# Optimization experiments

Hardware: AMD Instinct MI355X
Metric: run time of the kernel (lower is better)

## Reference

```python
import jax, jax.numpy as jnp
import numpy as np

CHW = (1, 256, 256)
NPH, NPW = 16, 16
NB = 8          # n_blocks
D = 384         # hidden_d
H = 6           # n_heads
DH = D // H     # d_head = 64
OUT = 4
PH, PW = CHW[1] // NPH, CHW[2] // NPW
IN_D = CHW[0] * PH * PW        # 256
S = NPH * NPW + 1              # 257 tokens (CLS + patches)
EPS = 1e-5                     # torch LayerNorm default


def positional_embeddings(seq_len, d):
    # matches get_positional_embeddings: sin(i/10000^(j/d)) even j, cos(i/10000^((j-1)/d)) odd j
    i = jnp.arange(seq_len, dtype=jnp.float32)[:, None]
    j = jnp.arange(d, dtype=jnp.float32)[None, :]
    j_eff = jnp.where(j % 2 == 0, j, j - 1)
    ang = i / jnp.power(jnp.float32(10000.0), j_eff / d)
    return jnp.where(j % 2 == 0, jnp.sin(ang), jnp.cos(ang))


def patchify(images):
    # (n,c,h,w) -> (n, NPH*NPW, c*PH*PW), patch flattened channel-first like patch.flatten()
    n, c, h, w = images.shape
    x = images.reshape(n, c, NPH, PH, NPW, PW)
    x = x.transpose(0, 2, 4, 1, 3, 5)  # n, nph, npw, c, ph, pw
    return x.reshape(n, NPH * NPW, c * PH * PW)


def layernorm(x, g, b):
    mu = jnp.mean(x, axis=-1, keepdims=True)
    var = jnp.mean(jnp.square(x - mu), axis=-1, keepdims=True)
    return (x - mu) * jax.lax.rsqrt(var + EPS) * g + b


def mhsa(x, Wq, bq, Wk, bk, Wv, bv):
    # x: [B,S,D]; W*: [H,DH,DH] (torch Linear convention out=x@W.T+b), b*: [H,DH]
    B = x.shape[0]
    xh = x.reshape(B, S, H, DH)
    q = jnp.einsum('bshd,hed->bshe', xh, Wq) + bq
    k = jnp.einsum('bshd,hed->bshe', xh, Wk) + bk
    v = jnp.einsum('bshd,hed->bshe', xh, Wv) + bv
    scores = jnp.einsum('bqhe,bkhe->bhqk', q, k) / jnp.float32(DH) ** 0.5
    attn = jax.nn.softmax(scores, axis=-1)
    o = jnp.einsum('bhqk,bkhe->bqhe', attn, v)
    return o.reshape(B, S, D)


def setup_inputs() -> dict:
    key = jax.random.key(0)
    ks = jax.random.split(key, 24)
    s = 0.02
    B = 64
    inp = {
        'images': jax.random.normal(ks[0], (B, *CHW), jnp.float32),
        'Wmap': jax.random.normal(ks[1], (D, IN_D), jnp.float32) * s,
        'bmap': jax.random.normal(ks[2], (D,), jnp.float32) * s,
        'cls': jax.random.uniform(ks[3], (1, D), jnp.float32),
        'ln1_g': jnp.ones((NB, D), jnp.float32),
        'ln1_b': jnp.zeros((NB, D), jnp.float32),
        'Wq': jax.random.normal(ks[4], (NB, H, DH, DH), jnp.float32) * s,
        'bq': jax.random.normal(ks[5], (NB, H, DH), jnp.float32) * s,
        'Wk': jax.random.normal(ks[6], (NB, H, DH, DH), jnp.float32) * s,
        'bk': jax.random.normal(ks[7], (NB, H, DH), jnp.float32) * s,
        'Wv': jax.random.normal(ks[8], (NB, H, DH, DH), jnp.float32) * s,
        'bv': jax.random.normal(ks[9], (NB, H, DH), jnp.float32) * s,
        'ln2_g': jnp.ones((NB, D), jnp.float32),
        'ln2_b': jnp.zeros((NB, D), jnp.float32),
        'W1': jax.random.normal(ks[10], (NB, 4 * D, D), jnp.float32) * s,
        'b1': jax.random.normal(ks[11], (NB, 4 * D), jnp.float32) * s,
        'W2': jax.random.normal(ks[12], (NB, D, 4 * D), jnp.float32) * s,
        'b2': jax.random.normal(ks[13], (NB, D), jnp.float32) * s,
        'Wout': jax.random.normal(ks[14], (OUT, D), jnp.float32) * s,
        'bout': jax.random.normal(ks[15], (OUT,), jnp.float32) * s,
    }
    return inp


def reference(images, Wmap, bmap, cls, ln1_g, ln1_b, Wq, bq, Wk, bk, Wv, bv,
              ln2_g, ln2_b, W1, b1, W2, b2, Wout, bout):
    B = images.shape[0]
    patches = patchify(images)                        # [B, S-1, IN_D]
    tokens = patches @ Wmap.T + bmap                  # [B, S-1, D]
    tokens = jnp.concatenate([jnp.broadcast_to(cls[None], (B, 1, D)), tokens], axis=1)
    out = tokens + positional_embeddings(S, D)[None]  # [B, S, D]
    for blk in range(NB):
        out = out + mhsa(layernorm(out, ln1_g[blk], ln1_b[blk]),
                         Wq[blk], bq[blk], Wk[blk], bk[blk], Wv[blk], bv[blk])
        h = layernorm(out, ln2_g[blk], ln2_b[blk])
        h = jax.nn.gelu(h @ W1[blk].T + b1[blk], approximate=False)
        out = out + (h @ W2[blk].T + b2[blk])
    cls_out = out[:, 0]                               # [B, D]
    return jax.nn.softmax(cls_out @ Wout.T + bout, axis=-1)
```

## Files before the change

kernel.cpp:

```cpp
#include <hip/hip_runtime.h>

typedef __bf16 bf16x8 __attribute__((ext_vector_type(8)));
typedef float f32x4 __attribute__((ext_vector_type(4)));
typedef unsigned short u16;
typedef unsigned short u16x4 __attribute__((ext_vector_type(4)));

typedef __attribute__((address_space(3))) unsigned int as3_u32;
typedef __attribute__((address_space(1))) unsigned int as1_u32;

static __device__ __forceinline__ float b2f(u16 u) {
    union { unsigned int ui; float f; } v; v.ui = ((unsigned int)u) << 16; return v.f;
}
static __device__ __forceinline__ u16 f2b(float f) {
    union { float f; unsigned int u; } v; v.f = f;
    unsigned int r = v.u + 0x7FFFu + ((v.u >> 16) & 1u);
    return (u16)(r >> 16);
}
static __device__ __forceinline__ float pos_emb(int s, int d) {
    int je = d & ~1;
    float ang = (float)s * powf(10000.0f, -(float)je / 384.0f);
    return (d & 1) ? cosf(ang) : sinf(ang);
}
static __device__ __forceinline__ float gelu_f(float x) {
    float xs = x * 0.70710678118654752f;
    float ax = fabsf(xs);
    float t = __builtin_amdgcn_rcpf(1.0f + 0.3275911f * ax);
    float poly = ((((1.061405429f * t - 1.453152027f) * t + 1.421413741f) * t
                   - 0.284496736f) * t + 0.254829592f) * t;
    float e = __expf(-ax * ax);
    float erfv = 1.0f - poly * e;
    erfv = (xs < 0.f) ? -erfv : erfv;
    return 0.5f * x * (1.0f + erfv);
}
static __device__ __forceinline__ void async16(const void* g, void* l) {
    __builtin_amdgcn_global_load_lds((const as1_u32*)g, (as3_u32*)l, 16, 0, 0);
}

#define MFMA16 __builtin_amdgcn_mfma_f32_16x16x32_bf16

template<int K>
static __device__ __forceinline__ void stage_tile(const u16* __restrict__ gbase,
                                                  u16* lds, int kt, int t) {
#pragma unroll
    for (int j = 0; j < 4; j++) {
        int o = j * 4096 + t * 16;
        int row = o >> 7;
        int c = (o >> 4) & 7;
        int gc = c ^ (row & 7);
        const u16* src = gbase + (size_t)row * K + kt * 64 + gc * 8;
        async16(src, (char*)lds + o);
    }
}

template<int K, int EPI>
__global__ __launch_bounds__(256) void k_gemm128(const u16* __restrict__ A,
                                                 const u16* __restrict__ Bw,
                                                 const float* __restrict__ bias,
                                                 u16* __restrict__ out16,
                                                 float* __restrict__ xres,
                                                 int m0g) {
    __shared__ u16 lds[2][128 * 64];
    const int t = threadIdx.x;
    const int NY = gridDim.y;
    int nwg = gridDim.x * NY;
    int flat = blockIdx.x + gridDim.x * blockIdx.y;
    int q8 = nwg >> 3, r8 = nwg & 7, xcd = flat & 7, idx = flat >> 3;
    int wg = (xcd < r8 ? xcd * (q8 + 1) : r8 * (q8 + 1) + (xcd - r8) * q8) + idx;
    const int mt = wg / NY, nt = wg - mt * NY;

    const u16* Ab = A + (size_t)mt * 128 * K;
    const u16* Bb = Bw + (size_t)nt * 128 * K;
    constexpr int NKT = K / 64;
    const int lane = t & 63, w = t >> 6;
    const int wm = (w >> 1) * 64, wn = (w & 1) * 64;
    const int r = lane & 15, g = lane >> 4;

    f32x4 acc[4][4] = {};
    for (int kt = 0; kt < NKT; kt++) {
        stage_tile<K>(Ab, lds[0], kt, t);
        stage_tile<K>(Bb, lds[1], kt, t);
        asm volatile("s_waitcnt vmcnt(0)" ::: "memory");
        __builtin_amdgcn_sched_barrier(0);
        __builtin_amdgcn_s_barrier();
        __builtin_amdgcn_sched_barrier(0);
#pragma unroll
        for (int ks = 0; ks < 2; ks++) {
            bf16x8 a[4], b[4];
#pragma unroll
            for (int i = 0; i < 4; i++) {
                int ra = wm + i * 16 + r;
                int ca = (ks * 4 + g) ^ (ra & 7);
                a[i] = *(const bf16x8*)((const char*)lds[0] + ra * 128 + ca * 16);
                int rb = wn + i * 16 + r;
                int cb = (ks * 4 + g) ^ (rb & 7);
                b[i] = *(const bf16x8*)((const char*)lds[1] + rb * 128 + cb * 16);
            }
            __builtin_amdgcn_s_setprio(1);
#pragma unroll
            for (int i = 0; i < 4; i++)
#pragma unroll
                for (int jj = 0; jj < 4; jj++)
                    acc[i][jj] = MFMA16(a[i], b[jj], acc[i][jj], 0, 0, 0);
            __builtin_amdgcn_s_setprio(0);
        }
        __builtin_amdgcn_s_barrier();
    }
#pragma unroll
    for (int i = 0; i < 4; i++) {
#pragma unroll
        for (int q = 0; q < 4; q++) {
            int ml = mt * 128 + wm + i * 16 + g * 4 + q;
#pragma unroll
            for (int jj = 0; jj < 4; jj++) {
                int n = nt * 128 + wn + jj * 16 + r;
                float v = acc[i][jj][q] + bias[n];
                if (EPI == 0) {
                    out16[(size_t)ml * 1536 + n] = f2b(gelu_f(v));
                } else {
                    int m = m0g + ml;
                    if (m < 16448) xres[(size_t)m * 384 + n] += v;
                }
            }
        }
    }
}

__global__ __launch_bounds__(64) void k_fattn(const u16* __restrict__ qb,
                                              const u16* __restrict__ kb,
                                              const u16* __restrict__ vT,
                                              float* __restrict__ x) {
    __shared__ u16 pl[32][40];
    const int lane = threadIdx.x;
    int flat = blockIdx.x;
    int xcd = flat & 7, idx = flat >> 3;
    int lbh = idx / 9;
    const int bh = xcd * 48 + lbh;
    const int q0 = (idx - lbh * 9) * 32;
    const int b = bh / 6, h = bh - b * 6;
    const int r = lane & 15, g = lane >> 4;

    const u16* qbase = qb + ((size_t)b * 257) * 384 + h * 64;
    const u16* kbase = kb + ((size_t)b * 257) * 384 + h * 64;
    const u16* vbase = vT + ((size_t)bh * 64) * 288;

    bf16x8 qf[2][2];
#pragma unroll
    for (int ti = 0; ti < 2; ti++)
#pragma unroll
        for (int kh = 0; kh < 2; kh++)
            qf[ti][kh] = *(const bf16x8*)(qbase + (size_t)(q0 + ti * 16 + r) * 384 + kh * 32 + g * 8);

    f32x4 accO[2][2][2] = {};
    f32x4 sum_[2] = {};

    for (int kv0 = 0; kv0 < 288; kv0 += 32) {
        bf16x8 kf[2][2];
#pragma unroll
        for (int tj = 0; tj < 2; tj++)
#pragma unroll
            for (int kh = 0; kh < 2; kh++)
                kf[tj][kh] = *(const bf16x8*)(kbase + (size_t)(kv0 + tj * 16 + r) * 384 + kh * 32 + g * 8);
        bf16x8 vf[2][2];
#pragma unroll
        for (int eT = 0; eT < 2; eT++)
#pragma unroll
            for (int tjE = 0; tjE < 2; tjE++)
                vf[eT][tjE] = *(const bf16x8*)(vbase + (size_t)(eT * 32 + tjE * 16 + r) * 288 + kv0 + g * 8);

        f32x4 s_[2][2] = {};
#pragma unroll
        for (int ti = 0; ti < 2; ti++)
#pragma unroll
            for (int tj = 0; tj < 2; tj++) {
                s_[ti][tj] = MFMA16(qf[ti][0], kf[tj][0], s_[ti][tj], 0, 0, 0);
                s_[ti][tj] = MFMA16(qf[ti][1], kf[tj][1], s_[ti][tj], 0, 0, 0);
            }
#pragma unroll
        for (int ti = 0; ti < 2; ti++) {
#pragma unroll
            for (int tj = 0; tj < 2; tj++) {
                bool bad = (kv0 + tj * 16 + r) >= 257;
#pragma unroll
                for (int q = 0; q < 4; q++) {
                    float p = bad ? 0.f : __expf(s_[ti][tj][q] * 0.125f);
                    s_[ti][tj][q] = p;
                }
                sum_[ti] += s_[ti][tj];
#pragma unroll
                for (int q = 0; q < 4; q++)
                    pl[ti * 16 + g * 4 + q][tj * 16 + r] = f2b(s_[ti][tj][q]);
            }
        }
        bf16x8 pa[2];
#pragma unroll
        for (int ti2 = 0; ti2 < 2; ti2++)
            pa[ti2] = *(const bf16x8*)&pl[ti2 * 16 + r][g * 8];
#pragma unroll
        for (int eT = 0; eT < 2; eT++)
#pragma unroll
            for (int ti2 = 0; ti2 < 2; ti2++)
#pragma unroll
                for (int tjE = 0; tjE < 2; tjE++)
                    accO[eT][ti2][tjE] = MFMA16(pa[ti2], vf[eT][tjE], accO[eT][ti2][tjE], 0, 0, 0);
    }
#pragma unroll
    for (int o = 1; o < 16; o <<= 1)
#pragma unroll
        for (int ti = 0; ti < 2; ti++)
#pragma unroll
            for (int q = 0; q < 4; q++)
                sum_[ti][q] += __shfl_xor(sum_[ti][q], o, 64);
#pragma unroll
    for (int ti = 0; ti < 2; ti++)
#pragma unroll
        for (int q = 0; q < 4; q++) {
            int qi = q0 + ti * 16 + g * 4 + q;
            if (qi < 257) {
                float inv = 1.0f / sum_[ti][q];
                float* px = x + ((size_t)b * 257 + qi) * 384 + h * 64;
#pragma unroll
                for (int eT = 0; eT < 2; eT++)
#pragma unroll
                    for (int tjE = 0; tjE < 2; tjE++)
                        px[eT * 32 + tjE * 16 + r] += accO[eT][ti][tjE][q] * inv;
            }
        }
}

__global__ __launch_bounds__(256) void k_cvt16(const void* __restrict__ src, u16* __restrict__ dst,
                                               int n, const unsigned* __restrict__ probe) {
    const bool isf32 = (*probe == 0x3F800000u);
    int i0 = (blockIdx.x * 256 + threadIdx.x) * 4;
    if (isf32) {
        const float* s = (const float*)src;
#pragma unroll
        for (int j = 0; j < 4; j++) { int i = i0 + j; if (i < n) dst[i] = f2b(s[i]); }
    } else {
        const u16* s = (const u16*)src;
#pragma unroll
        for (int j = 0; j < 4; j++) { int i = i0 + j; if (i < n) dst[i] = s[i]; }
    }
}
__global__ __launch_bounds__(256) void k_cvt32(const void* __restrict__ src, float* __restrict__ dst,
                                               int n, const unsigned* __restrict__ probe) {
    const bool isf32 = (*probe == 0x3F800000u);
    int i0 = (blockIdx.x * 256 + threadIdx.x) * 4;
    if (isf32) {
        const float* s = (const float*)src;
#pragma unroll
        for (int j = 0; j < 4; j++) { int i = i0 + j; if (i < n) dst[i] = s[i]; }
    } else {
        const u16* s = (const u16*)src;
#pragma unroll
        for (int j = 0; j < 4; j++) { int i = i0 + j; if (i < n) dst[i] = b2f(s[i]); }
    }
}

__global__ __launch_bounds__(256) void k_vtpad(u16* __restrict__ vT) {
    int idx = blockIdx.x * 256 + threadIdx.x;
    const int total = 384 * 64 * 31;
    if (idx < total) {
        int be = idx / 31; int s = 257 + (idx - be * 31);
        vT[(size_t)be * 288 + s] = 0;
    }
}

__global__ __launch_bounds__(256) void k_patch(const u16* __restrict__ img,
                                               const u16* __restrict__ Wmap,
                                               const float* __restrict__ bmap,
                                               float* __restrict__ x) {
    const int lane = threadIdx.x & 63;
    const int wv = threadIdx.x >> 6;
    const int mt = blockIdx.x * 4 + wv;
    const int nt = blockIdx.y;
    const int m0 = mt * 32, n0 = nt * 32;
    const int r = lane & 15, kr = (lane >> 4) << 3;
    f32x4 acc[2][2] = {};
    int ma = m0 + r;
    size_t base0 = (size_t)(ma >> 8) * 65536 + (size_t)((ma >> 4) & 15) * 4096 + (size_t)(ma & 15) * 16;
    ma += 16;
    size_t base1 = (size_t)(ma >> 8) * 65536 + (size_t)((ma >> 4) & 15) * 4096 + (size_t)(ma & 15) * 16;
    const u16* pb0 = Wmap + (size_t)(n0 + r) * 256 + kr;
    const u16* pb1 = pb0 + 16 * 256;
    for (int k0 = 0; k0 < 256; k0 += 32) {
        int k = k0 + kr;
        size_t off = (size_t)(k >> 4) * 256 + (k & 15);
        bf16x8 a0 = *(const bf16x8*)(img + base0 + off);
        bf16x8 a1 = *(const bf16x8*)(img + base1 + off);
        bf16x8 b0 = *(const bf16x8*)(pb0 + k0);
        bf16x8 b1 = *(const bf16x8*)(pb1 + k0);
        acc[0][0] = MFMA16(a0, b0, acc[0][0], 0, 0, 0);
        acc[0][1] = MFMA16(a0, b1, acc[0][1], 0, 0, 0);
        acc[1][0] = MFMA16(a1, b0, acc[1][0], 0, 0, 0);
        acc[1][1] = MFMA16(a1, b1, acc[1][1], 0, 0, 0);
    }
#pragma unroll
    for (int ti = 0; ti < 2; ti++)
#pragma unroll
        for (int i = 0; i < 4; i++) {
            int m = m0 + ti * 16 + ((lane >> 4) << 2) + i;
            int b = m >> 8, p = m & 255, s = p + 1;
            float* px = x + ((size_t)b * 257 + s) * 384;
#pragma unroll
            for (int tj = 0; tj < 2; tj++) {
                int n = n0 + tj * 16 + (lane & 15);
                px[n] = acc[ti][tj][i] + bmap[n] + pos_emb(s, n);
            }
        }
}

__global__ __launch_bounds__(384) void k_cls(const float* __restrict__ cls, float* __restrict__ x) {
    int b = blockIdx.x, d = threadIdx.x;
    x[(size_t)b * 257 * 384 + d] = cls[d] + pos_emb(0, d);
}

__global__ __launch_bounds__(256) void k_ln(const float* __restrict__ x,
                                            const float* __restrict__ g,
                                            const float* __restrict__ bb,
                                            u16* __restrict__ xn) {
    const int lane = threadIdx.x & 63, wv = threadIdx.x >> 6;
    const int row = blockIdx.x * 16 + wv * 4 + (lane >> 4);
    const int r = lane & 15;
    const float* px = x + (size_t)row * 384;
    f32x4 v[6]; float s = 0.f;
#pragma unroll
    for (int i = 0; i < 6; i++) {
        v[i] = *(const f32x4*)(px + i * 64 + r * 4);
        s += v[i][0] + v[i][1] + v[i][2] + v[i][3];
    }
#pragma unroll
    for (int o = 1; o < 16; o <<= 1) s += __shfl_xor(s, o, 64);
    float mu = s * (1.0f / 384.0f);
    float q = 0.f;
#pragma unroll
    for (int i = 0; i < 6; i++)
#pragma unroll
        for (int j = 0; j < 4; j++) { float d = v[i][j] - mu; q += d * d; }
#pragma unroll
    for (int o = 1; o < 16; o <<= 1) q += __shfl_xor(q, o, 64);
    float rstd = rsqrtf(q * (1.0f / 384.0f) + 1e-5f);
    u16* po = xn + (size_t)row * 384;
#pragma unroll
    for (int i = 0; i < 6; i++) {
        int d0 = i * 64 + r * 4;
        f32x4 gg = *(const f32x4*)(g + d0);
        f32x4 bv = *(const f32x4*)(bb + d0);
        u16x4 o4;
#pragma unroll
        for (int j = 0; j < 4; j++) o4[j] = f2b((v[i][j] - mu) * rstd * gg[j] + bv[j]);
        *(u16x4*)(po + d0) = o4;
    }
}

__global__ __launch_bounds__(256) void k_qkv3(const u16* __restrict__ xn,
                                              const u16* __restrict__ Wq,
                                              const u16* __restrict__ Wk,
                                              const u16* __restrict__ Wv,
                                              const float* __restrict__ bq,
                                              const float* __restrict__ bk,
                                              const float* __restrict__ bv,
                                              u16* __restrict__ qo,
                                              u16* __restrict__ ko,
                                              u16* __restrict__ vT) {
    const int lane = threadIdx.x & 63, wv = threadIdx.x >> 6;
    int nwg = 129 * 12;
    int flat = blockIdx.x + 129 * blockIdx.y;
    int q8 = nwg >> 3, r8 = nwg & 7, xcd = flat & 7, idx = flat >> 3;
    int wg = (xcd < r8 ? xcd * (q8 + 1) : r8 * (q8 + 1) + (xcd - r8) * q8) + idx;
    int bxx = wg / 12, rest = wg - bxx * 12;

    const int mt = bxx * 4 + wv; if (mt >= 514) return;
    const int nt = rest & 1, h = rest >> 1;
    const int r = lane & 15, kr = (lane >> 4) << 3;

    const u16* Abase = xn + (size_t)(mt * 32) * 384 + h * 64;
    bf16x8 a00 = *(const bf16x8*)(Abase + (size_t)r * 384 + kr);
    bf16x8 a10 = *(const bf16x8*)(Abase + (size_t)(16 + r) * 384 + kr);
    bf16x8 a01 = *(const bf16x8*)(Abase + (size_t)r * 384 + 32 + kr);
    bf16x8 a11 = *(const bf16x8*)(Abase + (size_t)(16 + r) * 384 + 32 + kr);

    const u16* Ws[3] = { Wq, Wk, Wv };
    const float* bs[3] = { bq, bk, bv };
#pragma unroll
    for (int ty = 0; ty < 3; ty++) {
        const u16* Bb = Ws[ty] + ((size_t)h * 64 + nt * 32) * 64;
        bf16x8 b00 = *(const bf16x8*)(Bb + (size_t)r * 64 + kr);
        bf16x8 b10 = *(const bf16x8*)(Bb + (size_t)(16 + r) * 64 + kr);
        bf16x8 b01 = *(const bf16x8*)(Bb + (size_t)r * 64 + 32 + kr);
        bf16x8 b11 = *(const bf16x8*)(Bb + (size_t)(16 + r) * 64 + 32 + kr);
        f32x4 acc[2][2] = {};
        acc[0][0] = MFMA16(a00, b00, acc[0][0], 0, 0, 0);
        acc[0][1] = MFMA16(a00, b10, acc[0][1], 0, 0, 0);
        acc[1][0] = MFMA16(a10, b00, acc[1][0], 0, 0, 0);
        acc[1][1] = MFMA16(a10, b10, acc[1][1], 0, 0, 0);
        acc[0][0] = MFMA16(a01, b01, acc[0][0], 0, 0, 0);
        acc[0][1] = MFMA16(a01, b11, acc[0][1], 0, 0, 0);
        acc[1][0] = MFMA16(a11, b01, acc[1][0], 0, 0, 0);
        acc[1][1] = MFMA16(a11, b11, acc[1][1], 0, 0, 0);
        const float* bias = bs[ty];
#pragma unroll
        for (int ti = 0; ti < 2; ti++)
#pragma unroll
            for (int i = 0; i < 4; i++) {
                int m = mt * 32 + ti * 16 + ((lane >> 4) << 2) + i;
#pragma unroll
                for (int tj = 0; tj < 2; tj++) {
                    int nl = nt * 32 + tj * 16 + (lane & 15);
                    float v = acc[ti][tj][i] + bias[h * 64 + nl];
                    if (ty == 0) {
                        qo[(size_t)m * 384 + h * 64 + nl] = f2b(v);
                    } else if (ty == 1) {
                        ko[(size_t)m * 384 + h * 64 + nl] = f2b(v);
                    } else {
                        int b = m / 257, s = m - b * 257;
                        vT[(((size_t)b * 6 + h) * 64 + nl) * 288 + s] = f2b(v);
                    }
                }
            }
    }
}

__global__ __launch_bounds__(256) void k_head(const float* __restrict__ x,
                                              const float* __restrict__ Wout,
                                              const float* __restrict__ bout,
                                              float* __restrict__ out) {
    int t = threadIdx.x; int b = t >> 2, o = t & 3;
    const float* px = x + (size_t)b * 257 * 384;
    const float* pw = Wout + o * 384;
    float s = 0.f;
    for (int d = 0; d < 384; d++) s += px[d] * pw[d];
    s += bout[o];
    float mx = fmaxf(s, __shfl_xor(s, 1, 4));
    mx = fmaxf(mx, __shfl_xor(mx, 2, 4));
    float e = expf(s - mx);
    float sm = e + __shfl_xor(e, 1, 4);
    sm += __shfl_xor(sm, 2, 4);
    out[t] = e / sm;
}

extern "C" void kernel_launch(void* const* d_in, const int* in_sizes, int n_in,
                              void* d_out, int out_size, void* d_ws, size_t ws_size,
                              hipStream_t stream) {
    const unsigned* probe = (const unsigned*)d_in[4];

    char* w = (char*)d_ws;
    size_t used = 0;
    auto alloc = [&](size_t bytes) -> char* {
        char* p = w + used; used += (bytes + 255) & ~(size_t)255; return p;
    };
    float* x   = (float*)alloc(16448ull * 384 * 4);
    u16*   xn  = (u16*)  alloc(16512ull * 384 * 2);
    u16*   qb  = (u16*)  alloc((16448ull + 32) * 384 * 2);
    u16*   kb  = (u16*)  alloc((16448ull + 32) * 384 * 2);
    u16*   vT  = (u16*)  alloc(384ull * 64 * 288 * 2);
    u16*   imB = (u16*)  alloc(4194304ull * 2);
    u16*   WmB = (u16*)  alloc(98304ull * 2);
    u16*   WqB = (u16*)  alloc(196608ull * 2);
    u16*   WkB = (u16*)  alloc(196608ull * 2);
    u16*   WvB = (u16*)  alloc(196608ull * 2);
    u16*   W1B = (u16*)  alloc(4718592ull * 2);
    u16*   W2B = (u16*)  alloc(4718592ull * 2);
    float* prm = (float*)alloc(39172ull * 4);
    char*  flexp = w + used;
    size_t flex = (ws_size > used) ? (ws_size - used) : 0;

    long long ft = (long long)(flex / (128ull * 1536 * 2));
    int FT128 = (ft > 129) ? 129 : (int)ft;
    if (FT128 < 1) FT128 = 1;
    u16* hb = (u16*)flexp;

    float* bmapF = prm + 0;
    float* clsF  = prm + 384;
    float* ln1gF = prm + 768;
    float* ln1bF = prm + 3840;
    float* bqF   = prm + 6912;
    float* bkF   = prm + 9984;
    float* bvF   = prm + 13056;
    float* ln2gF = prm + 16128;
    float* ln2bF = prm + 19200;
    float* b1F   = prm + 22272;
    float* b2F   = prm + 34560;
    float* WoutF = prm + 37632;
    float* boutF = prm + 39168;

    dim3 B256(256);
    auto cvt16 = [&](const void* src, u16* dst, int n) {
        hipLaunchKernelGGL(k_cvt16, dim3((n + 1023) / 1024), B256, 0, stream, src, dst, n, probe);
    };
    auto cvt32 = [&](const void* src, float* dst, int n) {
        hipLaunchKernelGGL(k_cvt32, dim3((n + 1023) / 1024), B256, 0, stream, src, dst, n, probe);
    };
    cvt16(d_in[0],  imB, 4194304);
    cvt16(d_in[1],  WmB, 98304);
    cvt16(d_in[6],  WqB, 196608);
    cvt16(d_in[8],  WkB, 196608);
    cvt16(d_in[10], WvB, 196608);
    cvt16(d_in[14], W1B, 4718592);
    cvt16(d_in[16], W2B, 4718592);
    cvt32(d_in[2],  bmapF, 384);
    cvt32(d_in[3],  clsF,  384);
    cvt32(d_in[4],  ln1gF, 3072);
    cvt32(d_in[5],  ln1bF, 3072);
    cvt32(d_in[7],  bqF,   3072);
    cvt32(d_in[9],  bkF,   3072);
    cvt32(d_in[11], bvF,   3072);
    cvt32(d_in[12], ln2gF, 3072);
    cvt32(d_in[13], ln2bF, 3072);
    cvt32(d_in[15], b1F,   12288);
    cvt32(d_in[17], b2F,   3072);
    cvt32(d_in[18], WoutF, 1536);
    cvt32(d_in[19], boutF, 4);
    (void)in_sizes; (void)n_in; (void)out_size;

    hipMemsetAsync(xn + 16448ull * 384, 0, 64ull * 384 * 2, stream);

    hipLaunchKernelGGL(k_vtpad, dim3((384 * 64 * 31 + 255) / 256), B256, 0, stream, vT);
    hipLaunchKernelGGL(k_patch, dim3(128, 12), B256, 0, stream, imB, WmB, bmapF, x);
    hipLaunchKernelGGL(k_cls, dim3(64), dim3(384), 0, stream, clsF, x);
    for (int blk = 0; blk < 8; blk++) {
        hipLaunchKernelGGL(k_ln, dim3(1028), B256, 0, stream, x, ln1gF + blk * 384, ln1bF + blk * 384, xn);
        hipLaunchKernelGGL(k_qkv3, dim3(129, 12), B256, 0, stream, xn,
                           WqB + (size_t)blk * 24576, WkB + (size_t)blk * 24576, WvB + (size_t)blk * 24576,
                           bqF + blk * 384, bkF + blk * 384, bvF + blk * 384,
                           qb, kb, vT);
        hipLaunchKernelGGL(k_fattn, dim3(3456), dim3(64), 0, stream, qb, kb, vT, x);
        hipLaunchKernelGGL(k_ln, dim3(1028), B256, 0, stream, x, ln2gF + blk * 384, ln2bF + blk * 384, xn);
        for (int T0 = 0; T0 < 129; T0 += FT128) {
            int nt = (129 - T0 < FT128) ? (129 - T0) : FT128;
            k_gemm128<384, 0><<<dim3(nt, 12), B256, 0, stream>>>(
                xn + (size_t)T0 * 128 * 384, W1B + (size_t)blk * 1536 * 384,
                b1F + blk * 1536, hb, nullptr, 0);
            k_gemm128<1536, 1><<<dim3(nt, 3), B256, 0, stream>>>(
                hb, W2B + (size_t)blk * 384 * 1536,
                b2F + blk * 384, nullptr, x, T0 * 128);
        }
    }
    hipLaunchKernelGGL(k_head, dim3(1), B256, 0, stream, x, WoutF, boutF, (float*)d_out);
}
```

Baseline: 1.401 ms.

## Enlarge MLP GEMM tiles to 256x128 with 512 threads and LDS-staged GELU stores

```diff
diff --git a/kernel.cpp b/kernel.cpp
--- a/kernel.cpp
+++ b/kernel.cpp
@@ -4,6 +4,7 @@
 typedef float f32x4 __attribute__((ext_vector_type(4)));
 typedef unsigned short u16;
 typedef unsigned short u16x4 __attribute__((ext_vector_type(4)));
+typedef unsigned short u16x8 __attribute__((ext_vector_type(8)));
 
 typedef __attribute__((address_space(3))) unsigned int as3_u32;
 typedef __attribute__((address_space(1))) unsigned int as1_u32;
@@ -38,28 +39,16 @@
 
 #define MFMA16 __builtin_amdgcn_mfma_f32_16x16x32_bf16
 
-template<int K>
-static __device__ __forceinline__ void stage_tile(const u16* __restrict__ gbase,
-                                                  u16* lds, int kt, int t) {
-#pragma unroll
-    for (int j = 0; j < 4; j++) {
-        int o = j * 4096 + t * 16;
-        int row = o >> 7;
-        int c = (o >> 4) & 7;
-        int gc = c ^ (row & 7);
-        const u16* src = gbase + (size_t)row * K + kt * 64 + gc * 8;
-        async16(src, (char*)lds + o);
-    }
-}
-
 template<int K, int EPI>
-__global__ __launch_bounds__(256) void k_gemm128(const u16* __restrict__ A,
+__global__ __launch_bounds__(512) void k_gemm256(const u16* __restrict__ A,
                                                  const u16* __restrict__ Bw,
                                                  const float* __restrict__ bias,
                                                  u16* __restrict__ out16,
                                                  float* __restrict__ xres,
                                                  int m0g) {
-    __shared__ u16 lds[2][128 * 64];
+    __shared__ u16 lds[24576];
+    u16* ldsA = lds;
+    u16* ldsB = lds + 16384;
     const int t = threadIdx.x;
     const int NY = gridDim.y;
     int nwg = gridDim.x * NY;
@@ -68,7 +57,7 @@
     int wg = (xcd < r8 ? xcd * (q8 + 1) : r8 * (q8 + 1) + (xcd - r8) * q8) + idx;
     const int mt = wg / NY, nt = wg - mt * NY;
 
-    const u16* Ab = A + (size_t)mt * 128 * K;
+    const u16* Ab = A + (size_t)mt * 256 * K;
     const u16* Bb = Bw + (size_t)nt * 128 * K;
     constexpr int NKT = K / 64;
     const int lane = t & 63, w = t >> 6;
@@ -77,8 +66,18 @@
 
     f32x4 acc[4][4] = {};
     for (int kt = 0; kt < NKT; kt++) {
-        stage_tile<K>(Ab, lds[0], kt, t);
-        stage_tile<K>(Bb, lds[1], kt, t);
+#pragma unroll
+        for (int j = 0; j < 4; j++) {
+            int o = j * 8192 + t * 16;
+            int row = o >> 7, c = (o >> 4) & 7, gc = c ^ (row & 7);
+            async16(Ab + (size_t)row * K + kt * 64 + gc * 8, (char*)ldsA + o);
+        }
+#pragma unroll
+        for (int j = 0; j < 2; j++) {
+            int o = j * 8192 + t * 16;
+            int row = o >> 7, c = (o >> 4) & 7, gc = c ^ (row & 7);
+            async16(Bb + (size_t)row * K + kt * 64 + gc * 8, (char*)ldsB + o);
+        }
         asm volatile("s_waitcnt vmcnt(0)" ::: "memory");
         __builtin_amdgcn_sched_barrier(0);
         __builtin_amdgcn_s_barrier();
@@ -90,10 +89,10 @@
             for (int i = 0; i < 4; i++) {
                 int ra = wm + i * 16 + r;
                 int ca = (ks * 4 + g) ^ (ra & 7);
-                a[i] = *(const bf16x8*)((const char*)lds[0] + ra * 128 + ca * 16);
+                a[i] = *(const bf16x8*)((const char*)ldsA + ra * 128 + ca * 16);
                 int rb = wn + i * 16 + r;
                 int cb = (ks * 4 + g) ^ (rb & 7);
-                b[i] = *(const bf16x8*)((const char*)lds[1] + rb * 128 + cb * 16);
+                b[i] = *(const bf16x8*)((const char*)ldsB + rb * 128 + cb * 16);
             }
             __builtin_amdgcn_s_setprio(1);
 #pragma unroll
@@ -105,21 +104,52 @@
         }
         __builtin_amdgcn_s_barrier();
     }
-#pragma unroll
-    for (int i = 0; i < 4; i++) {
-#pragma unroll
-        for (int q = 0; q < 4; q++) {
-            int ml = mt * 128 + wm + i * 16 + g * 4 + q;
-#pragma unroll
-            for (int jj = 0; jj < 4; jj++) {
-                int n = nt * 128 + wn + jj * 16 + r;
-                float v = acc[i][jj][q] + bias[n];
-                if (EPI == 0) {
-                    out16[(size_t)ml * 1536 + n] = f2b(gelu_f(v));
-                } else {
-                    int m = m0g + ml;
-                    if (m < 16448) xres[(size_t)m * 384 + n] += v;
+
+    if (EPI == 1) {
+#pragma unroll
+        for (int i = 0; i < 4; i++)
+#pragma unroll
+            for (int q = 0; q < 4; q++) {
+                int ml = mt * 256 + wm + i * 16 + g * 4 + q;
+                int m = m0g + ml;
+                if (m < 16448) {
+#pragma unroll
+                    for (int jj = 0; jj < 4; jj++) {
+                        int n = nt * 128 + wn + jj * 16 + r;
+                        xres[(size_t)m * 384 + n] += acc[i][jj][q] + bias[n];
+                    }
                 }
+            }
+    } else {
+#pragma unroll
+        for (int hi = 0; hi < 2; hi++) {
+            __syncthreads();
+            if ((w >> 2) == hi) {
+                int lwm = wm - hi * 128;
+#pragma unroll
+                for (int i = 0; i < 4; i++)
+#pragma unroll
+                    for (int q = 0; q < 4; q++) {
+                        int lr = lwm + i * 16 + g * 4 + q;
+                        int xorv = (lr & 12) << 3;
+#pragma unroll
+                        for (int jj = 0; jj < 4; jj++) {
+                            int col = wn + jj * 16 + r;
+                            float v = acc[i][jj][q] + bias[nt * 128 + col];
+                            *(u16*)((char*)lds + lr * 256 + ((col * 2) ^ xorv)) =
+                                f2b(gelu_f(v));
+                        }
+                    }
+            }
+            __syncthreads();
+            int prow = t >> 2;
+            int off = (t & 3) * 64;
+            int xorv = (prow & 12) << 3;
+            size_t gbase = (size_t)(mt * 256 + hi * 128 + prow) * 1536 + nt * 128 + off / 2;
+#pragma unroll
+            for (int k2 = 0; k2 < 4; k2++) {
+                u16x8 val = *(const u16x8*)((const char*)lds + prow * 256 + ((off + 16 * k2) ^ xorv));
+                *(u16x8*)(out16 + gbase + 8 * k2) = val;
             }
         }
     }
@@ -449,7 +479,7 @@
         char* p = w + used; used += (bytes + 255) & ~(size_t)255; return p;
     };
     float* x   = (float*)alloc(16448ull * 384 * 4);
-    u16*   xn  = (u16*)  alloc(16512ull * 384 * 2);
+    u16*   xn  = (u16*)  alloc(16640ull * 384 * 2);
     u16*   qb  = (u16*)  alloc((16448ull + 32) * 384 * 2);
     u16*   kb  = (u16*)  alloc((16448ull + 32) * 384 * 2);
     u16*   vT  = (u16*)  alloc(384ull * 64 * 288 * 2);
@@ -464,9 +494,9 @@
     char*  flexp = w + used;
     size_t flex = (ws_size > used) ? (ws_size - used) : 0;
 
-    long long ft = (long long)(flex / (128ull * 1536 * 2));
-    int FT128 = (ft > 129) ? 129 : (int)ft;
-    if (FT128 < 1) FT128 = 1;
+    long long ft = (long long)(flex / (256ull * 1536 * 2));
+    int FT256 = (ft > 65) ? 65 : (int)ft;
+    if (FT256 < 1) FT256 = 1;
     u16* hb = (u16*)flexp;
 
     float* bmapF = prm + 0;
@@ -512,7 +542,7 @@
     cvt32(d_in[19], boutF, 4);
     (void)in_sizes; (void)n_in; (void)out_size;
 
-    hipMemsetAsync(xn + 16448ull * 384, 0, 64ull * 384 * 2, stream);
+    hipMemsetAsync(xn + 16448ull * 384, 0, 192ull * 384 * 2, stream);
 
     hipLaunchKernelGGL(k_vtpad, dim3((384 * 64 * 31 + 255) / 256), B256, 0, stream, vT);
     hipLaunchKernelGGL(k_patch, dim3(128, 12), B256, 0, stream, imB, WmB, bmapF, x);
@@ -525,14 +555,14 @@
                            qb, kb, vT);
         hipLaunchKernelGGL(k_fattn, dim3(3456), dim3(64), 0, stream, qb, kb, vT, x);
         hipLaunchKernelGGL(k_ln, dim3(1028), B256, 0, stream, x, ln2gF + blk * 384, ln2bF + blk * 384, xn);
-        for (int T0 = 0; T0 < 129; T0 += FT128) {
-            int nt = (129 - T0 < FT128) ? (129 - T0) : FT128;
-            k_gemm128<384, 0><<<dim3(nt, 12), B256, 0, stream>>>(
-                xn + (size_t)T0 * 128 * 384, W1B + (size_t)blk * 1536 * 384,
+        for (int T0 = 0; T0 < 65; T0 += FT256) {
+            int nt = (65 - T0 < FT256) ? (65 - T0) : FT256;
+            k_gemm256<384, 0><<<dim3(nt, 12), dim3(512), 0, stream>>>(
+                xn + (size_t)T0 * 256 * 384, W1B + (size_t)blk * 1536 * 384,
                 b1F + blk * 1536, hb, nullptr, 0);
-            k_gemm128<1536, 1><<<dim3(nt, 3), B256, 0, stream>>>(
+            k_gemm256<1536, 1><<<dim3(nt, 3), dim3(512), 0, stream>>>(
                 hb, W2B + (size_t)blk * 384 * 1536,
-                b2F + blk * 384, nullptr, x, T0 * 128);
+                b2F + blk * 384, nullptr, x, T0 * 256);
         }
     }
     hipLaunchKernelGGL(k_head, dim3(1), B256, 0, stream, x, WoutF, boutF, (float*)d_out);
```

Result: slower. 1.532 ms (+9.3%).

## Fuse FFN up-projection, GELU and down-projection into one kernel

Applied to the files above, without the earlier changes.

```diff
diff --git a/kernel.cpp b/kernel.cpp
--- a/kernel.cpp
+++ b/kernel.cpp
@@ -38,91 +38,104 @@
 
 #define MFMA16 __builtin_amdgcn_mfma_f32_16x16x32_bf16
 
-template<int K>
-static __device__ __forceinline__ void stage_tile(const u16* __restrict__ gbase,
-                                                  u16* lds, int kt, int t) {
-#pragma unroll
-    for (int j = 0; j < 4; j++) {
-        int o = j * 4096 + t * 16;
-        int row = o >> 7;
-        int c = (o >> 4) & 7;
+__global__ __launch_bounds__(512) void k_ffn(const u16* __restrict__ xn,
+                                             const u16* __restrict__ W1,
+                                             const u16* __restrict__ W2,
+                                             const float* __restrict__ b1,
+                                             const float* __restrict__ b2,
+                                             float* __restrict__ x) {
+    __shared__ u16 lds[32768];
+    u16* hbl = lds + 24576;
+    const int t = threadIdx.x;
+    const int lane = t & 63, w = t >> 6;
+    const int r = lane & 15, g = lane >> 4;
+    const int m0 = blockIdx.x * 64;
+    const int hn = w * 16;
+    const int wn2 = w * 48;
+
+    const u16* xg = xn + (size_t)m0 * 384;
+#pragma unroll
+    for (int j = 0; j < 6; j++) {
+        int o = j * 8192 + t * 16;
+        int kt = o >> 13, rem = o & 8191;
+        int row = rem >> 7, c = (rem >> 4) & 7;
         int gc = c ^ (row & 7);
-        const u16* src = gbase + (size_t)row * K + kt * 64 + gc * 8;
-        async16(src, (char*)lds + o);
-    }
-}
-
-template<int K, int EPI>
-__global__ __launch_bounds__(256) void k_gemm128(const u16* __restrict__ A,
-                                                 const u16* __restrict__ Bw,
-                                                 const float* __restrict__ bias,
-                                                 u16* __restrict__ out16,
-                                                 float* __restrict__ xres,
-                                                 int m0g) {
-    __shared__ u16 lds[2][128 * 64];
-    const int t = threadIdx.x;
-    const int NY = gridDim.y;
-    int nwg = gridDim.x * NY;
-    int flat = blockIdx.x + gridDim.x * blockIdx.y;
-    int q8 = nwg >> 3, r8 = nwg & 7, xcd = flat & 7, idx = flat >> 3;
-    int wg = (xcd < r8 ? xcd * (q8 + 1) : r8 * (q8 + 1) + (xcd - r8) * q8) + idx;
-    const int mt = wg / NY, nt = wg - mt * NY;
-
-    const u16* Ab = A + (size_t)mt * 128 * K;
-    const u16* Bb = Bw + (size_t)nt * 128 * K;
-    constexpr int NKT = K / 64;
-    const int lane = t & 63, w = t >> 6;
-    const int wm = (w >> 1) * 64, wn = (w & 1) * 64;
-    const int r = lane & 15, g = lane >> 4;
-
-    f32x4 acc[4][4] = {};
-    for (int kt = 0; kt < NKT; kt++) {
-        stage_tile<K>(Ab, lds[0], kt, t);
-        stage_tile<K>(Bb, lds[1], kt, t);
-        asm volatile("s_waitcnt vmcnt(0)" ::: "memory");
+        async16(xg + (size_t)row * 384 + kt * 64 + gc * 8, (char*)lds + o);
+    }
+    asm volatile("s_waitcnt vmcnt(0)" ::: "memory");
+    __builtin_amdgcn_sched_barrier(0);
+    __builtin_amdgcn_s_barrier();
+
+    f32x4 acc2[4][3] = {};
+    for (int c = 0; c < 12; c++) {
+        f32x4 acc1[4] = {};
+        const u16* W1r = W1 + (size_t)(c * 128 + hn + r) * 384;
+#pragma unroll
+        for (int ks = 0; ks < 12; ks++) {
+            int kt = ks >> 1, k4 = (ks & 1) * 4;
+            bf16x8 bfrag = *(const bf16x8*)(W1r + ks * 32 + g * 8);
+#pragma unroll
+            for (int i = 0; i < 4; i++) {
+                int row = i * 16 + r;
+                int cc = (k4 + g) ^ (row & 7);
+                bf16x8 a = *(const bf16x8*)((const char*)lds + kt * 8192 + row * 128 + cc * 16);
+                acc1[i] = MFMA16(a, bfrag, acc1[i], 0, 0, 0);
+            }
+        }
+        __builtin_amdgcn_s_barrier();
+        {
+            float b1v = b1[c * 128 + hn + r];
+            int c6 = (hn + r) & 63;
+            int ktH = (hn + r) >> 6;
+            int cbase = ktH * 8192 + (c6 & 7) * 2;
+            int lc6 = c6 >> 3;
+#pragma unroll
+            for (int i = 0; i < 4; i++)
+#pragma unroll
+                for (int q = 0; q < 4; q++) {
+                    int hrow = i * 16 + g * 4 + q;
+                    float v = gelu_f(acc1[i][q] + b1v);
+                    int addr = cbase + hrow * 128 + ((lc6 ^ (hrow & 7)) << 4);
+                    *(u16*)((char*)hbl + addr) = f2b(v);
+                }
+        }
+        asm volatile("s_waitcnt lgkmcnt(0)" ::: "memory");
         __builtin_amdgcn_sched_barrier(0);
         __builtin_amdgcn_s_barrier();
-        __builtin_amdgcn_sched_barrier(0);
-#pragma unroll
-        for (int ks = 0; ks < 2; ks++) {
-            bf16x8 a[4], b[4];
+#pragma unroll
+        for (int kk = 0; kk < 4; kk++) {
+            int ktH = kk >> 1, k4 = (kk & 1) * 4;
+            bf16x8 a2[4];
 #pragma unroll
             for (int i = 0; i < 4; i++) {
-                int ra = wm + i * 16 + r;
-                int ca = (ks * 4 + g) ^ (ra & 7);
-                a[i] = *(const bf16x8*)((const char*)lds[0] + ra * 128 + ca * 16);
-                int rb = wn + i * 16 + r;
-                int cb = (ks * 4 + g) ^ (rb & 7);
-                b[i] = *(const bf16x8*)((const char*)lds[1] + rb * 128 + cb * 16);
-            }
-            __builtin_amdgcn_s_setprio(1);
-#pragma unroll
-            for (int i = 0; i < 4; i++)
-#pragma unroll
-                for (int jj = 0; jj < 4; jj++)
-                    acc[i][jj] = MFMA16(a[i], b[jj], acc[i][jj], 0, 0, 0);
-            __builtin_amdgcn_s_setprio(0);
-        }
-        __builtin_amdgcn_s_barrier();
-    }
-#pragma unroll
-    for (int i = 0; i < 4; i++) {
+                int row = i * 16 + r;
+                int cc = (k4 + g) ^ (row & 7);
+                a2[i] = *(const bf16x8*)((const char*)hbl + ktH * 8192 + row * 128 + cc * 16);
+            }
+#pragma unroll
+            for (int jj = 0; jj < 3; jj++) {
+                bf16x8 bf2 = *(const bf16x8*)(W2 + (size_t)(wn2 + jj * 16 + r) * 1536
+                                              + c * 128 + kk * 32 + g * 8);
+#pragma unroll
+                for (int i = 0; i < 4; i++)
+                    acc2[i][jj] = MFMA16(a2[i], bf2, acc2[i][jj], 0, 0, 0);
+            }
+        }
+    }
+#pragma unroll
+    for (int i = 0; i < 4; i++)
 #pragma unroll
         for (int q = 0; q < 4; q++) {
-            int ml = mt * 128 + wm + i * 16 + g * 4 + q;
-#pragma unroll
-            for (int jj = 0; jj < 4; jj++) {
-                int n = nt * 128 + wn + jj * 16 + r;
-                float v = acc[i][jj][q] + bias[n];
-                if (EPI == 0) {
-                    out16[(size_t)ml * 1536 + n] = f2b(gelu_f(v));
-                } else {
-                    int m = m0g + ml;
-                    if (m < 16448) xres[(size_t)m * 384 + n] += v;
+            int m = m0 + i * 16 + g * 4 + q;
+            if (m < 16448) {
+                float* px = x + (size_t)m * 384;
+#pragma unroll
+                for (int jj = 0; jj < 3; jj++) {
+                    int n = wn2 + jj * 16 + r;
+                    px[n] += acc2[i][jj][q] + b2[n];
                 }
             }
         }
-    }
 }
 
 __global__ __launch_bounds__(64) void k_fattn(const u16* __restrict__ qb,
@@ -449,7 +462,7 @@
         char* p = w + used; used += (bytes + 255) & ~(size_t)255; return p;
     };
     float* x   = (float*)alloc(16448ull * 384 * 4);
-    u16*   xn  = (u16*)  alloc(16512ull * 384 * 2);
+    u16*   xn  = (u16*)  alloc(16640ull * 384 * 2);
     u16*   qb  = (u16*)  alloc((16448ull + 32) * 384 * 2);
     u16*   kb  = (u16*)  alloc((16448ull + 32) * 384 * 2);
     u16*   vT  = (u16*)  alloc(384ull * 64 * 288 * 2);
@@ -461,13 +474,7 @@
     u16*   W1B = (u16*)  alloc(4718592ull * 2);
     u16*   W2B = (u16*)  alloc(4718592ull * 2);
     float* prm = (float*)alloc(39172ull * 4);
-    char*  flexp = w + used;
-    size_t flex = (ws_size > used) ? (ws_size - used) : 0;
-
-    long long ft = (long long)(flex / (128ull * 1536 * 2));
-    int FT128 = (ft > 129) ? 129 : (int)ft;
-    if (FT128 < 1) FT128 = 1;
-    u16* hb = (u16*)flexp;
+    (void)ws_size;
 
     float* bmapF = prm + 0;
     float* clsF  = prm + 384;
@@ -512,7 +519,7 @@
     cvt32(d_in[19], boutF, 4);
     (void)in_sizes; (void)n_in; (void)out_size;
 
-    hipMemsetAsync(xn + 16448ull * 384, 0, 64ull * 384 * 2, stream);
+    hipMemsetAsync(xn + 16448ull * 384, 0, 192ull * 384 * 2, stream);
 
     hipLaunchKernelGGL(k_vtpad, dim3((384 * 64 * 31 + 255) / 256), B256, 0, stream, vT);
     hipLaunchKernelGGL(k_patch, dim3(128, 12), B256, 0, stream, imB, WmB, bmapF, x);
@@ -525,15 +532,9 @@
                            qb, kb, vT);
         hipLaunchKernelGGL(k_fattn, dim3(3456), dim3(64), 0, stream, qb, kb, vT, x);
         hipLaunchKernelGGL(k_ln, dim3(1028), B256, 0, stream, x, ln2gF + blk * 384, ln2bF + blk * 384, xn);
-        for (int T0 = 0; T0 < 129; T0 += FT128) {
-            int nt = (129 - T0 < FT128) ? (129 - T0) : FT128;
-            k_gemm128<384, 0><<<dim3(nt, 12), B256, 0, stream>>>(
-                xn + (size_t)T0 * 128 * 384, W1B + (size_t)blk * 1536 * 384,
-                b1F + blk * 1536, hb, nullptr, 0);
-            k_gemm128<1536, 1><<<dim3(nt, 3), B256, 0, stream>>>(
-                hb, W2B + (size_t)blk * 384 * 1536,
-                b2F + blk * 384, nullptr, x, T0 * 128);
-        }
+        hipLaunchKernelGGL(k_ffn, dim3(258), dim3(512), 0, stream,
+                           xn, W1B + (size_t)blk * 1536 * 384, W2B + (size_t)blk * 384 * 1536,
+                           b1F + blk * 1536, b2F + blk * 384, x);
     }
     hipLaunchKernelGGL(k_head, dim3(1), B256, 0, stream, x, WoutF, boutF, (float*)d_out);
 }
```

Result: slower. 1.970 ms (+40.6%).

## Fuse attention residual add into LN2 kernel and drop MLP chunking

Applied to the files above, without the earlier changes.

```diff
diff --git a/kernel.cpp b/kernel.cpp
--- a/kernel.cpp
+++ b/kernel.cpp
@@ -57,8 +57,7 @@
                                                  const u16* __restrict__ Bw,
                                                  const float* __restrict__ bias,
                                                  u16* __restrict__ out16,
-                                                 float* __restrict__ xres,
-                                                 int m0g) {
+                                                 float* __restrict__ xres) {
     __shared__ u16 lds[2][128 * 64];
     const int t = threadIdx.x;
     const int NY = gridDim.y;
@@ -117,8 +116,7 @@
                 if (EPI == 0) {
                     out16[(size_t)ml * 1536 + n] = f2b(gelu_f(v));
                 } else {
-                    int m = m0g + ml;
-                    if (m < 16448) xres[(size_t)m * 384 + n] += v;
+                    if (ml < 16448) xres[(size_t)ml * 384 + n] += v;
                 }
             }
         }
@@ -128,7 +126,7 @@
 __global__ __launch_bounds__(64) void k_fattn(const u16* __restrict__ qb,
                                               const u16* __restrict__ kb,
                                               const u16* __restrict__ vT,
-                                              float* __restrict__ x) {
+                                              u16* __restrict__ ao) {
     __shared__ u16 pl[32][40];
     const int lane = threadIdx.x;
     int flat = blockIdx.x;
@@ -217,12 +215,12 @@
             int qi = q0 + ti * 16 + g * 4 + q;
             if (qi < 257) {
                 float inv = 1.0f / sum_[ti][q];
-                float* px = x + ((size_t)b * 257 + qi) * 384 + h * 64;
+                u16* pao = ao + ((size_t)b * 257 + qi) * 384 + h * 64;
 #pragma unroll
                 for (int eT = 0; eT < 2; eT++)
 #pragma unroll
                     for (int tjE = 0; tjE < 2; tjE++)
-                        px[eT * 32 + tjE * 16 + r] += accO[eT][ti][tjE][q] * inv;
+                        pao[eT * 32 + tjE * 16 + r] = f2b(accO[eT][ti][tjE][q] * inv);
             }
         }
 }
@@ -352,6 +350,50 @@
     }
 }
 
+__global__ __launch_bounds__(256) void k_ln2r(float* __restrict__ x,
+                                              const u16* __restrict__ ao,
+                                              const float* __restrict__ g,
+                                              const float* __restrict__ bb,
+                                              u16* __restrict__ xn) {
+    const int lane = threadIdx.x & 63, wv = threadIdx.x >> 6;
+    const int row = blockIdx.x * 16 + wv * 4 + (lane >> 4);
+    const int r = lane & 15;
+    float* px = x + (size_t)row * 384;
+    const u16* pa = ao + (size_t)row * 384;
+    f32x4 v[6]; float s = 0.f;
+#pragma unroll
+    for (int i = 0; i < 6; i++) {
+        v[i] = *(const f32x4*)(px + i * 64 + r * 4);
+        u16x4 a4 = *(const u16x4*)(pa + i * 64 + r * 4);
+#pragma unroll
+        for (int j = 0; j < 4; j++) v[i][j] += b2f(a4[j]);
+        s += v[i][0] + v[i][1] + v[i][2] + v[i][3];
+    }
+#pragma unroll
+    for (int o = 1; o < 16; o <<= 1) s += __shfl_xor(s, o, 64);
+    float mu = s * (1.0f / 384.0f);
+    float q = 0.f;
+#pragma unroll
+    for (int i = 0; i < 6; i++)
+#pragma unroll
+        for (int j = 0; j < 4; j++) { float d = v[i][j] - mu; q += d * d; }
+#pragma unroll
+    for (int o = 1; o < 16; o <<= 1) q += __shfl_xor(q, o, 64);
+    float rstd = rsqrtf(q * (1.0f / 384.0f) + 1e-5f);
+    u16* po = xn + (size_t)row * 384;
+#pragma unroll
+    for (int i = 0; i < 6; i++) {
+        int d0 = i * 64 + r * 4;
+        *(f32x4*)(px + d0) = v[i];
+        f32x4 gg = *(const f32x4*)(g + d0);
+        f32x4 bv = *(const f32x4*)(bb + d0);
+        u16x4 o4;
+#pragma unroll
+        for (int j = 0; j < 4; j++) o4[j] = f2b((v[i][j] - mu) * rstd * gg[j] + bv[j]);
+        *(u16x4*)(po + d0) = o4;
+    }
+}
+
 __global__ __launch_bounds__(256) void k_qkv3(const u16* __restrict__ xn,
                                               const u16* __restrict__ Wq,
                                               const u16* __restrict__ Wk,
@@ -453,6 +495,7 @@
     u16*   qb  = (u16*)  alloc((16448ull + 32) * 384 * 2);
     u16*   kb  = (u16*)  alloc((16448ull + 32) * 384 * 2);
     u16*   vT  = (u16*)  alloc(384ull * 64 * 288 * 2);
+    u16*   ao  = (u16*)  alloc(16448ull * 384 * 2);
     u16*   imB = (u16*)  alloc(4194304ull * 2);
     u16*   WmB = (u16*)  alloc(98304ull * 2);
     u16*   WqB = (u16*)  alloc(196608ull * 2);
@@ -461,13 +504,8 @@
     u16*   W1B = (u16*)  alloc(4718592ull * 2);
     u16*   W2B = (u16*)  alloc(4718592ull * 2);
     float* prm = (float*)alloc(39172ull * 4);
-    char*  flexp = w + used;
-    size_t flex = (ws_size > used) ? (ws_size - used) : 0;
-
-    long long ft = (long long)(flex / (128ull * 1536 * 2));
-    int FT128 = (ft > 129) ? 129 : (int)ft;
-    if (FT128 < 1) FT128 = 1;
-    u16* hb = (u16*)flexp;
+    u16*   hb  = (u16*)  alloc(16512ull * 1536 * 2);
+    (void)ws_size;
 
     float* bmapF = prm + 0;
     float* clsF  = prm + 384;
@@ -523,17 +561,13 @@
                            WqB + (size_t)blk * 24576, WkB + (size_t)blk * 24576, WvB + (size_t)blk * 24576,
                            bqF + blk * 384, bkF + blk * 384, bvF + blk * 384,
                            qb, kb, vT);
-        hipLaunchKernelGGL(k_fattn, dim3(3456), dim3(64), 0, stream, qb, kb, vT, x);
-        hipLaunchKernelGGL(k_ln, dim3(1028), B256, 0, stream, x, ln2gF + blk * 384, ln2bF + blk * 384, xn);
-        for (int T0 = 0; T0 < 129; T0 += FT128) {
-            int nt = (129 - T0 < FT128) ? (129 - T0) : FT128;
-            k_gemm128<384, 0><<<dim3(nt, 12), B256, 0, stream>>>(
-                xn + (size_t)T0 * 128 * 384, W1B + (size_t)blk * 1536 * 384,
-                b1F + blk * 1536, hb, nullptr, 0);
-            k_gemm128<1536, 1><<<dim3(nt, 3), B256, 0, stream>>>(
-                hb, W2B + (size_t)blk * 384 * 1536,
-                b2F + blk * 384, nullptr, x, T0 * 128);
-        }
+        hipLaunchKernelGGL(k_fattn, dim3(3456), dim3(64), 0, stream, qb, kb, vT, ao);
+        hipLaunchKernelGGL(k_ln2r, dim3(1028), B256, 0, stream, x, ao,
+                           ln2gF + blk * 384, ln2bF + blk * 384, xn);
+        k_gemm128<384, 0><<<dim3(129, 12), B256, 0, stream>>>(
+            xn, W1B + (size_t)blk * 1536 * 384, b1F + blk * 1536, hb, nullptr);
+        k_gemm128<1536, 1><<<dim3(129, 3), B256, 0, stream>>>(
+            hb, W2B + (size_t)blk * 384 * 1536, b2F + blk * 384, nullptr, x);
     }
     hipLaunchKernelGGL(k_head, dim3(1), B256, 0, stream, x, WoutF, boutF, (float*)d_out);
 }
```

New measurement: 1.398 ms. Within noise of the previous version (-0.3%).
